# Optimization experiments

Measured on AMD Instinct MI355X. Metric: run time of the kernel, lower is better.

Reference implementation:

```python
import jax, jax.numpy as jnp
import numpy as np

H = 12  # num_attention_heads
DH = 64  # attention_head_size


def setup_inputs() -> dict:
    key = jax.random.key(0)
    ks = jax.random.split(key, 4)
    B, S, D = 2, 2048, 768
    sc = 1.0 / np.sqrt(D)
    return {
        "hidden_states": jax.random.normal(ks[0], (B, S, D), jnp.float32),
        "attention_mask": jnp.zeros((B, 1, 1, S), jnp.float32),
        "Wq": jax.random.normal(ks[1], (D, D), jnp.float32) * sc,
        "bq": jnp.zeros((D,), jnp.float32),
        "Wk": jax.random.normal(ks[2], (D, D), jnp.float32) * sc,
        "bk": jnp.zeros((D,), jnp.float32),
        "Wv": jax.random.normal(ks[3], (D, D), jnp.float32) * sc,
        "bv": jnp.zeros((D,), jnp.float32),
    }


def reference(hidden_states, attention_mask, Wq, bq, Wk, bk, Wv, bv):
    B, S, D = hidden_states.shape
    # Linear projections (nn.Linear: x @ W^T + b); weights stored here as [in, out]
    q = hidden_states @ Wq + bq
    k = hidden_states @ Wk + bk
    v = hidden_states @ Wv + bv
    # [B, S, D] -> [B, H, S, Dh]
    def split_heads(x):
        return x.reshape(B, S, H, DH).transpose(0, 2, 1, 3)
    q, k, v = split_heads(q), split_heads(k), split_heads(v)
    scores = jnp.einsum("bhqd,bhkd->bhqk", q, k) / jnp.sqrt(jnp.float32(DH))
    scores = scores + attention_mask  # broadcast [B,1,1,S] additive mask
    attention_softmax = jax.nn.softmax(scores, axis=-1)
    # dropout is identity in eval mode
    context = jnp.einsum("bhqk,bhkd->bhqd", attention_softmax, v)
    context = context.transpose(0, 2, 1, 3).reshape(B, S, H * DH)
    return (context, attention_softmax)
```

## Files before the change

### kernel.cpp

```cpp
#include <hip/hip_runtime.h>
#include <hip/hip_bf16.h>

#define S_LEN 2048
#define DM 768
#define NH 12
#define DH 64
#define BATCH 2
#define SC 0.1803368801111204f
#define LOG2E 1.4426950408889634f

typedef __attribute__((ext_vector_type(8))) short bf16x8;
typedef __attribute__((ext_vector_type(4))) float f32x4;
typedef __attribute__((ext_vector_type(16))) float f32x16;
typedef __attribute__((ext_vector_type(8))) unsigned short u16x8;

__device__ __forceinline__ unsigned short f2bf(float f) {
  union { float f; unsigned u; } v; v.f = f;
  unsigned r = (v.u + 0x7fffu + ((v.u >> 16) & 1u)) >> 16;
  return (unsigned short)r;
}
__device__ __forceinline__ unsigned cvt2(float a, float b) {
  __hip_bfloat162 h = __float22bfloat162_rn(float2{a, b});
  return *reinterpret_cast<unsigned*>(&h);
}

__global__ __launch_bounds__(256) void wtrans(
    const float* __restrict__ Wq, const float* __restrict__ Wk, const float* __restrict__ Wv,
    unsigned short* __restrict__ Wt)
{
  const int z = blockIdx.z;
  const float* W = (z == 0) ? Wq : (z == 1) ? Wk : Wv;
  const float sc = (z == 0) ? SC : 1.0f;
  __shared__ float Lt[64][65];
  const int t = threadIdx.x;
  const int row0 = blockIdx.y * 64, col0 = blockIdx.x * 64;
  const int r = t >> 2, c0 = (t & 3) * 16;
  const float4* src = (const float4*)(W + (size_t)(row0 + r) * DM + col0 + c0);
  #pragma unroll
  for (int j = 0; j < 4; ++j) {
    const float4 v = src[j];
    Lt[r][c0 + 4 * j] = v.x; Lt[r][c0 + 4 * j + 1] = v.y;
    Lt[r][c0 + 4 * j + 2] = v.z; Lt[r][c0 + 4 * j + 3] = v.w;
  }
  __syncthreads();
  const int nn = t >> 2, kk0 = (t & 3) * 16;
  unsigned wo[8];
  #pragma unroll
  for (int j = 0; j < 8; ++j)
    wo[j] = cvt2(Lt[kk0 + 2 * j][nn] * sc, Lt[kk0 + 2 * j + 1][nn] * sc);
  unsigned short* dst = Wt + ((size_t)(z * DM + col0 + nn)) * DM + row0 + kk0;
  *(uint4*)dst = *(uint4*)&wo[0];
  *(uint4*)(dst + 8) = *(uint4*)&wo[4];
}

#define BM 128
#define BN 128
#define BK 64
#define LDPAD 72

__global__ __launch_bounds__(256) void qkv_gemm(
    const float* __restrict__ X,
    const unsigned short* __restrict__ Wt,
    const float* __restrict__ bq, const float* __restrict__ bk, const float* __restrict__ bv,
    unsigned short* __restrict__ Qo, unsigned short* __restrict__ Kf,
    unsigned short* __restrict__ Vf)
{
  const int z = blockIdx.z;
  const float* bias = (z == 0) ? bq : (z == 1) ? bk : bv;
  const float bsc = (z == 0) ? SC : 1.0f;

  __shared__ __align__(16) unsigned short Al[BM][LDPAD];
  __shared__ __align__(16) unsigned short Bl[BN][LDPAD];

  const int t = threadIdx.x;
  const int wv = t >> 6, lane = t & 63;
  const int g = lane >> 4, c = lane & 15;
  const int wm = (wv >> 1) * 64, wn = (wv & 1) * 64;
  const int m0 = blockIdx.y * BM, n0 = blockIdx.x * BN;

  f32x4 acc[4][4];
  #pragma unroll
  for (int i = 0; i < 4; ++i)
    #pragma unroll
    for (int j = 0; j < 4; ++j) {
      float bb = bias[n0 + wn + j * 16 + c] * bsc;
      f32x4 a4 = {bb, bb, bb, bb};
      acc[i][j] = a4;
    }

  const int a_m = t >> 1, a_k = (t & 1) * 32;

  for (int kt = 0; kt < DM / BK; ++kt) {
    const int k0 = kt * BK;
    __syncthreads();
    #pragma unroll
    for (int half = 0; half < 2; ++half) {
      const float4* src = (const float4*)(X + (size_t)(m0 + a_m) * DM + k0 + a_k + 16 * half);
      const float4 x0 = src[0], x1 = src[1], x2 = src[2], x3 = src[3];
      uint4 v0 = {cvt2(x0.x, x0.y), cvt2(x0.z, x0.w), cvt2(x1.x, x1.y), cvt2(x1.z, x1.w)};
      uint4 v1 = {cvt2(x2.x, x2.y), cvt2(x2.z, x2.w), cvt2(x3.x, x3.y), cvt2(x3.z, x3.w)};
      *(uint4*)&Al[a_m][a_k + 16 * half] = v0;
      *(uint4*)&Al[a_m][a_k + 16 * half + 8] = v1;
    }
    {
      const unsigned short* srcB = Wt + ((size_t)(z * DM + n0 + a_m)) * DM + k0 + a_k;
      const u16x8 w0 = *(const u16x8*)srcB;
      const u16x8 w1 = *(const u16x8*)(srcB + 8);
      const u16x8 w2 = *(const u16x8*)(srcB + 16);
      const u16x8 w3 = *(const u16x8*)(srcB + 24);
      *(u16x8*)&Bl[a_m][a_k] = w0;
      *(u16x8*)&Bl[a_m][a_k + 8] = w1;
      *(u16x8*)&Bl[a_m][a_k + 16] = w2;
      *(u16x8*)&Bl[a_m][a_k + 24] = w3;
    }
    __syncthreads();
    #pragma unroll
    for (int kk = 0; kk < 2; ++kk) {
      bf16x8 af[4], bfr[4];
      #pragma unroll
      for (int i = 0; i < 4; ++i) af[i]  = *(const bf16x8*)&Al[wm + i * 16 + c][kk * 32 + 8 * g];
      #pragma unroll
      for (int j = 0; j < 4; ++j) bfr[j] = *(const bf16x8*)&Bl[wn + j * 16 + c][kk * 32 + 8 * g];
      #pragma unroll
      for (int i = 0; i < 4; ++i)
        #pragma unroll
        for (int j = 0; j < 4; ++j)
          acc[i][j] = __builtin_amdgcn_mfma_f32_16x16x32_bf16(af[i], bfr[j], acc[i][j], 0, 0, 0);
    }
  }

  if (z == 0) {
    #pragma unroll
    for (int i = 0; i < 4; ++i)
      #pragma unroll
      for (int j = 0; j < 4; ++j)
        #pragma unroll
        for (int r = 0; r < 4; ++r) {
          const int m = m0 + wm + i * 16 + 4 * g + r;
          const int n = n0 + wn + j * 16 + c;
          Qo[(size_t)m * DM + n] = f2bf(acc[i][j][r]);
        }
  } else if (z == 1) {
    #pragma unroll
    for (int i = 0; i < 4; ++i)
      #pragma unroll
      for (int j = 0; j < 4; ++j) {
        const int n = n0 + wn + j * 16 + c;
        const int h = n >> 6, d = n & 63, ch = d >> 3, e = d & 7;
        #pragma unroll
        for (int r = 0; r < 4; ++r) {
          const int m = m0 + wm + i * 16 + 4 * g + r;
          const int b = m >> 11, s = m & 2047;
          const int st = s >> 5, r32 = s & 31;
          const size_t w = (((size_t)(b * NH + h) * 64 + st) * 8 + ch) * 32 + r32;
          Kf[w * 8 + e] = f2bf(acc[i][j][r]);
        }
      }
  } else {
    #pragma unroll
    for (int i = 0; i < 4; ++i)
      #pragma unroll
      for (int j = 0; j < 4; ++j) {
        const int n = n0 + wn + j * 16 + c;
        const int h = n >> 6, d = n & 63;
        const int mb = m0 + wm + i * 16 + 4 * g;
        const int b = mb >> 11, s = mb & 2047;
        const int kk = s >> 3, j0 = s & 7;
        unsigned short* dst = &Vf[(((size_t)(b * NH + h) * 256 + kk) * 64 + d) * 8 + j0];
        uint2 pk = {cvt2(acc[i][j][0], acc[i][j][1]), cvt2(acc[i][j][2], acc[i][j][3])};
        *(uint2*)dst = pk;
      }
  }
}

__global__ __launch_bounds__(256, 3) void attn_fused(
    const unsigned short* __restrict__ Qb,
    const bf16x8* __restrict__ Kf,
    const bf16x8* __restrict__ Vf,
    const float* __restrict__ mask,
    float* __restrict__ ctx,
    float* __restrict__ Pout)
{
  const int bid = blockIdx.x;
  const int wg = (bid & 7) * 192 + (bid >> 3);
  const int qt = wg & 63;
  const int bh = wg >> 6;
  const int b = bh / NH, h = bh % NH;

  const int t = threadIdx.x, wv = t >> 6, lane = t & 63;
  const int q = lane & 31, hi = lane >> 5;
  const int q0 = qt * 32;

  __shared__ __align__(16) float Pf[4][2][32][36];
  __shared__ __align__(16) float Osum[32][68];
  __shared__ float mlb[4][32];

  bf16x8 bqf[4];
  {
    const unsigned short* qp = Qb + (size_t)(b * S_LEN + q0 + q) * DM + h * DH + 8 * hi;
    #pragma unroll
    for (int m = 0; m < 4; ++m) bqf[m] = *(const bf16x8*)(qp + 16 * m);
  }

  const bf16x8* kfb = Kf + ((size_t)bh * 64 + wv * 16) * 256;
  const bf16x8* vfb = Vf + ((size_t)bh * 256 + wv * 64) * 64;
  const float* mrow = mask + (size_t)b * S_LEN + wv * 512;

  float ll = 0.f;

  bf16x8 kc[4];
  #pragma unroll
  for (int m = 0; m < 4; ++m) kc[m] = kfb[(2 * m + hi) * 32 + q];

  for (int st = 0; st < 16; ++st) {
    bf16x8 kn[4];
    const int stn = (st + 1) & 15;
    #pragma unroll
    for (int m = 0; m < 4; ++m) kn[m] = kfb[stn * 256 + (2 * m + hi) * 32 + q];

    f32x16 s;
    #pragma unroll
    for (int rg = 0; rg < 4; ++rg) {
      const f32x4 mk = *(const f32x4*)&mrow[st * 32 + 8 * rg + 4 * hi];
      #pragma unroll
      for (int ri = 0; ri < 4; ++ri) s[4 * rg + ri] = mk[ri] * LOG2E;
    }
    #pragma unroll
    for (int m = 0; m < 4; ++m)
      s = __builtin_amdgcn_mfma_f32_32x32x16_bf16(kc[m], bqf[m], s, 0, 0, 0);

    float e[16];
    #pragma unroll
    for (int r = 0; r < 16; ++r) e[r] = __builtin_amdgcn_exp2f(s[r]);
    const float t0 = (e[0] + e[1]) + (e[2] + e[3]);
    const float t1 = (e[4] + e[5]) + (e[6] + e[7]);
    const float t2 = (e[8] + e[9]) + (e[10] + e[11]);
    const float t3 = (e[12] + e[13]) + (e[14] + e[15]);
    ll += (t0 + t1) + (t2 + t3);
    #pragma unroll
    for (int m = 0; m < 4; ++m) kc[m] = kn[m];
  }
  ll += __shfl_xor(ll, 32);
  if (hi == 0) mlb[wv][q] = ll;
  __syncthreads();

  const float lsum = (mlb[0][q] + mlb[1][q]) + (mlb[2][q] + mlb[3][q]);
  const float mfin = __builtin_amdgcn_logf(lsum);

  f32x16 o0, o1;
  #pragma unroll
  for (int r = 0; r < 16; ++r) { o0[r] = 0.f; o1[r] = 0.f; }

  float* pbase = Pout + (size_t)bh * S_LEN * S_LEN + (size_t)q0 * S_LEN + wv * 512;
  const int sr = lane >> 3, scl = lane & 7;

  for (int st = 0; st < 16; ++st) {
    const int cur = st & 1;
    bf16x8 kn[4];
    const int stn = (st + 1) & 15;
    #pragma unroll
    for (int m = 0; m < 4; ++m) kn[m] = kfb[stn * 256 + (2 * m + hi) * 32 + q];

    const bf16x8 vb00 = vfb[(st * 4 + hi) * 64 + q];
    const bf16x8 vb01 = vfb[(st * 4 + hi) * 64 + 32 + q];
    const bf16x8 vb10 = vfb[(st * 4 + 2 + hi) * 64 + q];
    const bf16x8 vb11 = vfb[(st * 4 + 2 + hi) * 64 + 32 + q];

    f32x16 s;
    #pragma unroll
    for (int rg = 0; rg < 4; ++rg) {
      const f32x4 mk = *(const f32x4*)&mrow[st * 32 + 8 * rg + 4 * hi];
      #pragma unroll
      for (int ri = 0; ri < 4; ++ri) s[4 * rg + ri] = mk[ri] * LOG2E;
    }
    #pragma unroll
    for (int m = 0; m < 4; ++m)
      s = __builtin_amdgcn_mfma_f32_32x32x16_bf16(kc[m], bqf[m], s, 0, 0, 0);

    #pragma unroll
    for (int r = 0; r < 16; ++r) s[r] = __builtin_amdgcn_exp2f(s[r] - mfin);

    #pragma unroll
    for (int rg = 0; rg < 4; ++rg) {
      f32x4 pv = {s[4 * rg], s[4 * rg + 1], s[4 * rg + 2], s[4 * rg + 3]};
      *(f32x4*)&Pf[wv][cur][q][8 * rg + 4 * hi] = pv;
    }

    unsigned c0 = cvt2(s[0], s[1]),   c1 = cvt2(s[2], s[3]);
    unsigned c2 = cvt2(s[4], s[5]),   c3 = cvt2(s[6], s[7]);
    unsigned c4 = cvt2(s[8], s[9]),   c5 = cvt2(s[10], s[11]);
    unsigned c6 = cvt2(s[12], s[13]), c7 = cvt2(s[14], s[15]);
    auto r02 = __builtin_amdgcn_permlane32_swap(c0, c2, false, false);
    auto r13 = __builtin_amdgcn_permlane32_swap(c1, c3, false, false);
    auto r46 = __builtin_amdgcn_permlane32_swap(c4, c6, false, false);
    auto r57 = __builtin_amdgcn_permlane32_swap(c5, c7, false, false);
    uint4 u0 = {r02[0], r13[0], r02[1], r13[1]};
    uint4 u1 = {r46[0], r57[0], r46[1], r57[1]};
    const bf16x8 pa0 = *reinterpret_cast<bf16x8*>(&u0);
    const bf16x8 pa1 = *reinterpret_cast<bf16x8*>(&u1);

    o0 = __builtin_amdgcn_mfma_f32_32x32x16_bf16(pa0, vb00, o0, 0, 0, 0);
    o0 = __builtin_amdgcn_mfma_f32_32x32x16_bf16(pa1, vb10, o0, 0, 0, 0);
    o1 = __builtin_amdgcn_mfma_f32_32x32x16_bf16(pa0, vb01, o1, 0, 0, 0);
    o1 = __builtin_amdgcn_mfma_f32_32x32x16_bf16(pa1, vb11, o1, 0, 0, 0);

    if (st > 0) {
      float* pst = pbase + (st - 1) * 32;
      #pragma unroll
      for (int i = 0; i < 4; ++i) {
        const f32x4 row = *(const f32x4*)&Pf[wv][cur ^ 1][sr + 8 * i][scl * 4];
        *(f32x4*)(pst + (size_t)(sr + 8 * i) * S_LEN + scl * 4) = row;
      }
    }
    #pragma unroll
    for (int m = 0; m < 4; ++m) kc[m] = kn[m];
  }
  {
    float* pst = pbase + 15 * 32;
    #pragma unroll
    for (int i = 0; i < 4; ++i) {
      const f32x4 row = *(const f32x4*)&Pf[wv][1][sr + 8 * i][scl * 4];
      *(f32x4*)(pst + (size_t)(sr + 8 * i) * S_LEN + scl * 4) = row;
    }
  }

  #pragma unroll
  for (int w = 0; w < 4; ++w) {
    if (wv == w) {
      #pragma unroll
      for (int rg = 0; rg < 4; ++rg)
        #pragma unroll
        for (int ri = 0; ri < 4; ++ri) {
          const int qr = ri + 8 * rg + 4 * hi;
          if (w == 0) {
            Osum[qr][q]      = o0[4 * rg + ri];
            Osum[qr][32 + q] = o1[4 * rg + ri];
          } else {
            Osum[qr][q]      += o0[4 * rg + ri];
            Osum[qr][32 + q] += o1[4 * rg + ri];
          }
        }
    }
    __syncthreads();
  }

  const int row = t >> 3, d0 = (t & 7) * 8;
  const f32x4 r0 = *(const f32x4*)&Osum[row][d0];
  const f32x4 r1 = *(const f32x4*)&Osum[row][d0 + 4];
  float* crow = ctx + (size_t)(b * S_LEN + q0 + row) * DM + h * DH + d0;
  *(f32x4*)crow = r0;
  *(f32x4*)(crow + 4) = r1;
}

extern "C" void kernel_launch(void* const* d_in, const int* in_sizes, int n_in,
                              void* d_out, int out_size, void* d_ws, size_t ws_size,
                              hipStream_t stream) {
  const float* hs   = (const float*)d_in[0];
  const float* mask = (const float*)d_in[1];
  const float* Wq = (const float*)d_in[2];
  const float* bq = (const float*)d_in[3];
  const float* Wk = (const float*)d_in[4];
  const float* bk = (const float*)d_in[5];
  const float* Wv = (const float*)d_in[6];
  const float* bv = (const float*)d_in[7];

  const size_t MT = (size_t)BATCH * S_LEN * DM;
  unsigned short* Qb = (unsigned short*)d_ws;
  unsigned short* Kf = Qb + MT;
  unsigned short* Vf = Kf + MT;
  unsigned short* Wt = Vf + MT;

  float* ctx  = (float*)d_out;
  float* Pout = ctx + MT;

  wtrans<<<dim3(12, 12, 3), 256, 0, stream>>>(Wq, Wk, Wv, Wt);
  qkv_gemm<<<dim3(DM / BN, (BATCH * S_LEN) / BM, 3), 256, 0, stream>>>(
      hs, Wt, bq, bk, bv, Qb, Kf, Vf);
  attn_fused<<<dim3((S_LEN / 32) * NH * BATCH), 256, 0, stream>>>(
      Qb, (const bf16x8*)Kf, (const bf16x8*)Vf, mask, ctx, Pout);
}
```

Measured before the change: 176.8 us.

## Double-buffer QKV GEMM shared tiles and raise wave priority around attention MFMAs

The QKV projection GEMM now uses two shared-memory buffers. The next K-tile's global loads and bf16 conversion are prefetched into registers while MFMAs run on the current tile, which removes one barrier per iteration and overlaps memory latency with compute. Separately, the attention kernel wraps its MFMA groups in s_setprio(1)/s_setprio(0) so waves issuing matrix ops get scheduling priority over waves doing exp or stores. Costs are doubled LDS for the GEMM tiles and extra staging registers, which may reduce occupancy.

```diff
diff --git a/kernel.cpp b/kernel.cpp
--- a/kernel.cpp
+++ b/kernel.cpp
@@ -57,6 +57,7 @@
 #define BN 128
 #define BK 64
 #define LDPAD 72
+#define NKT (DM / BK)
 
 __global__ __launch_bounds__(256) void qkv_gemm(
     const float* __restrict__ X,
@@ -69,8 +70,8 @@
   const float* bias = (z == 0) ? bq : (z == 1) ? bk : bv;
   const float bsc = (z == 0) ? SC : 1.0f;
 
-  __shared__ __align__(16) unsigned short Al[BM][LDPAD];
-  __shared__ __align__(16) unsigned short Bl[BN][LDPAD];
+  __shared__ __align__(16) unsigned short Al[2][BM][LDPAD];
+  __shared__ __align__(16) unsigned short Bl[2][BN][LDPAD];
 
   const int t = threadIdx.x;
   const int wv = t >> 6, lane = t & 63;
@@ -90,43 +91,52 @@
 
   const int a_m = t >> 1, a_k = (t & 1) * 32;
 
-  for (int kt = 0; kt < DM / BK; ++kt) {
+  uint4 xa[4];
+  u16x8 wb[4];
+  auto stage_regs = [&](int kt) {
     const int k0 = kt * BK;
-    __syncthreads();
     #pragma unroll
     for (int half = 0; half < 2; ++half) {
       const float4* src = (const float4*)(X + (size_t)(m0 + a_m) * DM + k0 + a_k + 16 * half);
       const float4 x0 = src[0], x1 = src[1], x2 = src[2], x3 = src[3];
-      uint4 v0 = {cvt2(x0.x, x0.y), cvt2(x0.z, x0.w), cvt2(x1.x, x1.y), cvt2(x1.z, x1.w)};
-      uint4 v1 = {cvt2(x2.x, x2.y), cvt2(x2.z, x2.w), cvt2(x3.x, x3.y), cvt2(x3.z, x3.w)};
-      *(uint4*)&Al[a_m][a_k + 16 * half] = v0;
-      *(uint4*)&Al[a_m][a_k + 16 * half + 8] = v1;
-    }
-    {
-      const unsigned short* srcB = Wt + ((size_t)(z * DM + n0 + a_m)) * DM + k0 + a_k;
-      const u16x8 w0 = *(const u16x8*)srcB;
-      const u16x8 w1 = *(const u16x8*)(srcB + 8);
-      const u16x8 w2 = *(const u16x8*)(srcB + 16);
-      const u16x8 w3 = *(const u16x8*)(srcB + 24);
-      *(u16x8*)&Bl[a_m][a_k] = w0;
-      *(u16x8*)&Bl[a_m][a_k + 8] = w1;
-      *(u16x8*)&Bl[a_m][a_k + 16] = w2;
-      *(u16x8*)&Bl[a_m][a_k + 24] = w3;
-    }
-    __syncthreads();
+      xa[2 * half]     = uint4{cvt2(x0.x, x0.y), cvt2(x0.z, x0.w), cvt2(x1.x, x1.y), cvt2(x1.z, x1.w)};
+      xa[2 * half + 1] = uint4{cvt2(x2.x, x2.y), cvt2(x2.z, x2.w), cvt2(x3.x, x3.y), cvt2(x3.z, x3.w)};
+    }
+    const unsigned short* srcB = Wt + ((size_t)(z * DM + n0 + a_m)) * DM + k0 + a_k;
+    #pragma unroll
+    for (int j = 0; j < 4; ++j) wb[j] = *(const u16x8*)(srcB + 8 * j);
+  };
+  auto write_buf = [&](int buf) {
+    *(uint4*)&Al[buf][a_m][a_k]      = xa[0];
+    *(uint4*)&Al[buf][a_m][a_k + 8]  = xa[1];
+    *(uint4*)&Al[buf][a_m][a_k + 16] = xa[2];
+    *(uint4*)&Al[buf][a_m][a_k + 24] = xa[3];
+    #pragma unroll
+    for (int j = 0; j < 4; ++j) *(u16x8*)&Bl[buf][a_m][a_k + 8 * j] = wb[j];
+  };
+
+  stage_regs(0);
+  write_buf(0);
+  __syncthreads();
+
+  for (int kt = 0; kt < NKT; ++kt) {
+    const int cur = kt & 1;
+    if (kt + 1 < NKT) stage_regs(kt + 1);
     #pragma unroll
     for (int kk = 0; kk < 2; ++kk) {
       bf16x8 af[4], bfr[4];
       #pragma unroll
-      for (int i = 0; i < 4; ++i) af[i]  = *(const bf16x8*)&Al[wm + i * 16 + c][kk * 32 + 8 * g];
-      #pragma unroll
-      for (int j = 0; j < 4; ++j) bfr[j] = *(const bf16x8*)&Bl[wn + j * 16 + c][kk * 32 + 8 * g];
+      for (int i = 0; i < 4; ++i) af[i]  = *(const bf16x8*)&Al[cur][wm + i * 16 + c][kk * 32 + 8 * g];
+      #pragma unroll
+      for (int j = 0; j < 4; ++j) bfr[j] = *(const bf16x8*)&Bl[cur][wn + j * 16 + c][kk * 32 + 8 * g];
       #pragma unroll
       for (int i = 0; i < 4; ++i)
         #pragma unroll
         for (int j = 0; j < 4; ++j)
           acc[i][j] = __builtin_amdgcn_mfma_f32_16x16x32_bf16(af[i], bfr[j], acc[i][j], 0, 0, 0);
     }
+    if (kt + 1 < NKT) write_buf(cur ^ 1);
+    __syncthreads();
   }
 
   if (z == 0) {
@@ -225,9 +235,11 @@
       #pragma unroll
       for (int ri = 0; ri < 4; ++ri) s[4 * rg + ri] = mk[ri] * LOG2E;
     }
+    __builtin_amdgcn_s_setprio(1);
     #pragma unroll
     for (int m = 0; m < 4; ++m)
       s = __builtin_amdgcn_mfma_f32_32x32x16_bf16(kc[m], bqf[m], s, 0, 0, 0);
+    __builtin_amdgcn_s_setprio(0);
 
     float e[16];
     #pragma unroll
@@ -273,9 +285,11 @@
       #pragma unroll
       for (int ri = 0; ri < 4; ++ri) s[4 * rg + ri] = mk[ri] * LOG2E;
     }
+    __builtin_amdgcn_s_setprio(1);
     #pragma unroll
     for (int m = 0; m < 4; ++m)
       s = __builtin_amdgcn_mfma_f32_32x32x16_bf16(kc[m], bqf[m], s, 0, 0, 0);
+    __builtin_amdgcn_s_setprio(0);
 
     #pragma unroll
     for (int r = 0; r < 16; ++r) s[r] = __builtin_amdgcn_exp2f(s[r] - mfin);
@@ -299,10 +313,12 @@
     const bf16x8 pa0 = *reinterpret_cast<bf16x8*>(&u0);
     const bf16x8 pa1 = *reinterpret_cast<bf16x8*>(&u1);
 
+    __builtin_amdgcn_s_setprio(1);
     o0 = __builtin_amdgcn_mfma_f32_32x32x16_bf16(pa0, vb00, o0, 0, 0, 0);
     o0 = __builtin_amdgcn_mfma_f32_32x32x16_bf16(pa1, vb10, o0, 0, 0, 0);
     o1 = __builtin_amdgcn_mfma_f32_32x32x16_bf16(pa0, vb01, o1, 0, 0, 0);
     o1 = __builtin_amdgcn_mfma_f32_32x32x16_bf16(pa1, vb11, o1, 0, 0, 0);
+    __builtin_amdgcn_s_setprio(0);
 
     if (st > 0) {
       float* pst = pbase + (st - 1) * 32;
```

Measured after the change: 187.6 us. 1.06x slower.
